# Kernel optimization log

Measured on AMD Instinct MI355X. Metric: run time of the kernel, lower is better.

## Reference

```python
import jax, jax.numpy as jnp
import numpy as np

D_MODEL = 1024
D_HIDDEN = 4096
NUM_BANKS = 16
NUM_SELECTED = 2


def setup_inputs() -> dict:
    key = jax.random.key(0)
    ks = jax.random.split(key, 7)
    s = 0.02
    return {
        "tensor": jax.random.normal(ks[0], (4, 1024, D_MODEL), dtype=jnp.float32),
        "Wr": jax.random.normal(ks[1], (D_MODEL, NUM_BANKS), dtype=jnp.float32) * s,
        "br": jnp.zeros((NUM_BANKS,), dtype=jnp.float32),
        "W1": jax.random.normal(ks[2], (NUM_BANKS, D_MODEL, D_HIDDEN), dtype=jnp.float32) * s,
        "b1": jnp.zeros((NUM_BANKS, D_HIDDEN), dtype=jnp.float32),
        "W2": jax.random.normal(ks[3], (NUM_BANKS, D_HIDDEN, D_MODEL), dtype=jnp.float32) * s,
        "b2": jnp.zeros((NUM_BANKS, D_MODEL), dtype=jnp.float32),
    }


def reference(tensor, Wr, br, W1, b1, W2, b2):
    # Router: softmax over banks, keep top-k probabilities (BankSelector)
    logits = jnp.einsum("bsd,de->bse", tensor, Wr) + br          # [B,S,E]
    probs = jax.nn.softmax(logits, axis=-1)
    topv, topi = jax.lax.top_k(probs, NUM_SELECTED)              # [B,S,K]
    # Dense gate [B,S,E]: selected banks carry their router probability,
    # all other banks are zeroed (equivalent to sparse dispatch/combine).
    gate = jnp.sum(jax.nn.one_hot(topi, NUM_BANKS, dtype=tensor.dtype)
                   * topv[..., None], axis=-2)                    # [B,S,E]
    # Banked expert FFN (BankedLinear x2 with ReLU between)
    h = jax.nn.relu(jnp.einsum("bsd,edh->bseh", tensor, W1) + b1)  # [B,S,E,Dh]
    y = jnp.einsum("bseh,ehm->bsem", h, W2) + b2                   # [B,S,E,Dm]
    # Weighted combine across selected banks
    out = jnp.einsum("bse,bsem->bsm", gate, y)                     # [B,S,Dm]
    return out
```

## Files before the change

kernel.cpp:

```cpp
#include <hip/hip_runtime.h>
#include <stdint.h>

#define D_MODEL   1024
#define D_HIDDEN  4096
#define NBANKS    16
#define NTOK      4096

#define BM 128
#define BN 128
#define BK 32
#define TBUF (BM * BK)
#define KS2 4

typedef __attribute__((ext_vector_type(8))) short bf16x8;
typedef __attribute__((ext_vector_type(4))) float f32x4;
typedef __attribute__((ext_vector_type(4))) unsigned int u32x4;
typedef __attribute__((ext_vector_type(2))) unsigned int u32x2;

__device__ __forceinline__ unsigned short f2bf(float f) {
  unsigned u = __builtin_bit_cast(unsigned, f);
  u += 0x7FFFu + ((u >> 16) & 1u);
  return (unsigned short)(u >> 16);
}

__device__ __forceinline__ unsigned cvtpk(float lo, float hi) {
  unsigned r;
  asm("v_cvt_pk_bf16_f32 %0, %1, %2" : "=v"(r) : "v"(lo), "v"(hi));
  return r;
}

__device__ __forceinline__ int sidx(int r, int k) {
  return (r << 5) + ((((k >> 3) ^ ((r >> 2) & 3)) << 3) | (k & 7));
}

__global__ __launch_bounds__(256) void zero_out_k(float4* __restrict__ out4,
                                                  int* __restrict__ counts) {
  size_t i = (size_t)blockIdx.x * 256 + threadIdx.x;
  out4[i] = make_float4(0.f, 0.f, 0.f, 0.f);
  if (blockIdx.x == 0 && threadIdx.x < NBANKS) counts[threadIdx.x] = 0;
}

__global__ __launch_bounds__(256) void cvtx_k(const float* __restrict__ X,
                                              unsigned short* __restrict__ Xb) {
  const size_t i = ((size_t)blockIdx.x * 256 + threadIdx.x) * 8;
  const float4 a = *(const float4*)(X + i);
  const float4 b = *(const float4*)(X + i + 4);
  u32x4 v;
  v[0] = cvtpk(a.x, a.y); v[1] = cvtpk(a.z, a.w);
  v[2] = cvtpk(b.x, b.y); v[3] = cvtpk(b.z, b.w);
  *(u32x4*)(Xb + i) = v;
}

__global__ __launch_bounds__(64) void router_k(const float* __restrict__ x,
                                               const float* __restrict__ Wr,
                                               const float* __restrict__ br,
                                               int* __restrict__ topIdx,
                                               float* __restrict__ topGate) {
  const int t = blockIdx.x;
  const int l = threadIdx.x;
  const float* xr = x + (size_t)t * D_MODEL;

  float acc[NBANKS];
#pragma unroll
  for (int e = 0; e < NBANKS; ++e) acc[e] = 0.f;

  for (int d = l; d < D_MODEL; d += 64) {
    const float xv = xr[d];
    const float* wrow = Wr + (size_t)d * NBANKS;
#pragma unroll
    for (int e = 0; e < NBANKS; ++e) acc[e] += xv * wrow[e];
  }
#pragma unroll
  for (int e = 0; e < NBANKS; ++e) {
#pragma unroll
    for (int m = 1; m < 64; m <<= 1) acc[e] += __shfl_xor(acc[e], m, 64);
  }
#pragma unroll
  for (int e = 0; e < NBANKS; ++e) acc[e] += br[e];

  if (l == 0) {
    float mx = acc[0];
#pragma unroll
    for (int e = 1; e < NBANKS; ++e) mx = fmaxf(mx, acc[e]);
    float p[NBANKS];
    float s = 0.f;
#pragma unroll
    for (int e = 0; e < NBANKS; ++e) { p[e] = expf(acc[e] - mx); s += p[e]; }
    int i0 = 0; float v0 = p[0];
#pragma unroll
    for (int e = 1; e < NBANKS; ++e) if (p[e] > v0) { v0 = p[e]; i0 = e; }
    int i1 = -1; float v1 = -1.f;
#pragma unroll
    for (int e = 0; e < NBANKS; ++e) if (e != i0 && p[e] > v1) { v1 = p[e]; i1 = e; }
    const float inv = 1.f / s;
    topIdx[2 * t]     = i0;
    topIdx[2 * t + 1] = i1;
    topGate[2 * t]     = v0 * inv;
    topGate[2 * t + 1] = v1 * inv;
  }
}

__global__ __launch_bounds__(256) void build_lists_k(const int* __restrict__ topIdx,
                                                     const float* __restrict__ topGate,
                                                     int* __restrict__ counts,
                                                     int* __restrict__ rowlist,
                                                     float* __restrict__ gatelist) {
  const int t = blockIdx.x * 256 + threadIdx.x;
  if (t >= NTOK) return;
#pragma unroll
  for (int k = 0; k < 2; ++k) {
    const int e = topIdx[2 * t + k];
    const int p = atomicAdd(&counts[e], 1);
    rowlist[e * NTOK + p]  = t;
    gatelist[e * NTOK + p] = topGate[2 * t + k];
  }
}

__global__ void scan_k(const int* __restrict__ counts, int* __restrict__ bankOff) {
  if (threadIdx.x == 0) {
    int s = 0;
#pragma unroll
    for (int e = 0; e < NBANKS; ++e) { bankOff[e] = s; s += counts[e]; }
    bankOff[NBANKS] = s;
  }
}

__global__ __launch_bounds__(256, 2) void gemm1_k(const unsigned short* __restrict__ Xb,
                                                  const float* __restrict__ W1,
                                                  const float* __restrict__ b1,
                                                  const int* __restrict__ counts,
                                                  const int* __restrict__ bankOff,
                                                  const int* __restrict__ rowlist,
                                                  unsigned short* __restrict__ H) {
  const int e   = blockIdx.z;
  const int cnt = counts[e];
  const int m0  = blockIdx.y * BM;
  if (m0 >= cnt) return;
  const int n0  = blockIdx.x * BN;

  const int tid  = threadIdx.x;
  const int lane = tid & 63;
  const int w    = tid >> 6;
  const int wm   = (w >> 1) * 64;
  const int wn   = (w & 1) * 64;

  __shared__ unsigned short Xs[2 * TBUF];
  __shared__ unsigned short Ws[2 * TBUF];

  const int arow = tid >> 1;
  const int ak   = (tid & 1) * 16;
  const int gi   = min(m0 + arow, cnt - 1);
  const int tok  = rowlist[e * NTOK + gi];
  const unsigned short* Asrc = Xb + (size_t)tok * D_MODEL + ak;
  const int xo0 = sidx(arow, ak);
  const int xo1 = sidx(arow, ak + 8);

  const int n4 = 4 * (tid & 31);
  const int k4 = 4 * (tid >> 5);
  const float* Bsrc = W1 + (size_t)e * D_MODEL * D_HIDDEN + (size_t)k4 * D_HIDDEN + n0 + n4;
  int wo[4];
#pragma unroll
  for (int i = 0; i < 4; ++i) wo[i] = sidx(n4 + i, k4);

  const int fr = lane & 15;
  const int fc = (lane >> 4) * 8;
  int aoff[4], boff[4];
#pragma unroll
  for (int i = 0; i < 4; ++i) {
    aoff[i] = sidx(wm + i * 16 + fr, fc);
    boff[i] = sidx(wn + i * 16 + fr, fc);
  }

  bf16x8 ra0, ra1;
  float rbf[4][4];

  f32x4 acc[4][4];
#pragma unroll
  for (int i = 0; i < 4; ++i)
#pragma unroll
    for (int j = 0; j < 4; ++j)
#pragma unroll
      for (int r = 0; r < 4; ++r) acc[i][j][r] = 0.f;

  unsigned short* xc = &Xs[0];       unsigned short* wc = &Ws[0];
  unsigned short* xn = &Xs[TBUF];    unsigned short* wn_ = &Ws[TBUF];

  auto LOAD = [&](int t) {
    const unsigned short* ap = Asrc + t * BK;
    ra0 = *(const bf16x8*)(ap);
    ra1 = *(const bf16x8*)(ap + 8);
    const float* bp = Bsrc + (size_t)t * BK * D_HIDDEN;
#pragma unroll
    for (int kk = 0; kk < 4; ++kk)
      *(float4*)&rbf[kk][0] = *(const float4*)(bp + (size_t)kk * D_HIDDEN);
  };

  auto WRITE = [&](unsigned short* xs, unsigned short* ws) {
    *(bf16x8*)(xs + xo0) = ra0;
    *(bf16x8*)(xs + xo1) = ra1;
#pragma unroll
    for (int i = 0; i < 4; ++i) {
      u32x2 v;
      v[0] = cvtpk(rbf[0][i], rbf[1][i]);
      v[1] = cvtpk(rbf[2][i], rbf[3][i]);
      *(u32x2*)(ws + wo[i]) = v;
    }
  };

  auto COMPUTE = [&](const unsigned short* xs, const unsigned short* ws) {
    bf16x8 af[4], bb[4];
#pragma unroll
    for (int mb = 0; mb < 4; ++mb) af[mb] = *(const bf16x8*)(xs + aoff[mb]);
#pragma unroll
    for (int nb = 0; nb < 4; ++nb) bb[nb] = *(const bf16x8*)(ws + boff[nb]);
#pragma unroll
    for (int mb = 0; mb < 4; ++mb)
#pragma unroll
      for (int nb = 0; nb < 4; ++nb)
        acc[mb][nb] = __builtin_amdgcn_mfma_f32_16x16x32_bf16(af[mb], bb[nb], acc[mb][nb], 0, 0, 0);
  };

  const int NT = D_MODEL / BK;
  LOAD(0);
  WRITE(xc, wc);
  __syncthreads();
#pragma unroll 1
  for (int t = 0; t < NT; ++t) {
    if (t + 1 < NT) LOAD(t + 1);
    __builtin_amdgcn_sched_barrier(0);
    COMPUTE(xc, wc);
    if (t + 1 < NT) WRITE(xn, wn_);
    __syncthreads();
    unsigned short* t0 = xc; xc = xn;  xn  = t0;
    unsigned short* t1 = wc; wc = wn_; wn_ = t1;
  }

  const int hb = bankOff[e] + m0;
  const int rq = (lane >> 4) * 4;
#pragma unroll
  for (int nb = 0; nb < 4; ++nb) {
    const int col = n0 + wn + nb * 16 + fr;
    const float bias = b1[e * D_HIDDEN + col];
#pragma unroll
    for (int mb = 0; mb < 4; ++mb)
#pragma unroll
      for (int r = 0; r < 4; ++r) {
        const int rowT = wm + mb * 16 + rq + r;
        if (m0 + rowT < cnt) {
          float v = acc[mb][nb][r] + bias;
          v = fmaxf(v, 0.f);
          H[(size_t)(hb + rowT) * D_HIDDEN + col] = f2bf(v);
        }
      }
  }
}

__global__ __launch_bounds__(256, 2) void gemm2_k(const unsigned short* __restrict__ H,
                                                  const float* __restrict__ W2,
                                                  const float* __restrict__ b2,
                                                  const int* __restrict__ counts,
                                                  const int* __restrict__ bankOff,
                                                  const int* __restrict__ rowlist,
                                                  const float* __restrict__ gatelist,
                                                  float* __restrict__ out) {
  const int z   = blockIdx.z;
  const int e   = z >> 2;
  const int kc  = z & 3;
  const int cnt = counts[e];
  const int m0  = blockIdx.y * BM;
  if (m0 >= cnt) return;
  const int n0  = blockIdx.x * BN;
  const int kc0 = kc * (D_HIDDEN / KS2);

  const int tid  = threadIdx.x;
  const int lane = tid & 63;
  const int w    = tid >> 6;
  const int wm   = (w >> 1) * 64;
  const int wn   = (w & 1) * 64;

  __shared__ unsigned short Xs[2 * TBUF];
  __shared__ unsigned short Ws[2 * TBUF];

  const int arow = tid >> 1;
  const int ak   = (tid & 1) * 16;
  const int hb   = bankOff[e];
  const int gi   = hb + min(m0 + arow, cnt - 1);
  const unsigned short* Asrc = H + (size_t)gi * D_HIDDEN + kc0 + ak;
  const int xo0 = sidx(arow, ak);
  const int xo1 = sidx(arow, ak + 8);

  const int n4 = 4 * (tid & 31);
  const int k4 = 4 * (tid >> 5);
  const float* Bsrc = W2 + (size_t)e * D_HIDDEN * D_MODEL + (size_t)(kc0 + k4) * D_MODEL + n0 + n4;
  int wo[4];
#pragma unroll
  for (int i = 0; i < 4; ++i) wo[i] = sidx(n4 + i, k4);

  const int fr = lane & 15;
  const int fc = (lane >> 4) * 8;
  int aoff[4], boff[4];
#pragma unroll
  for (int i = 0; i < 4; ++i) {
    aoff[i] = sidx(wm + i * 16 + fr, fc);
    boff[i] = sidx(wn + i * 16 + fr, fc);
  }

  bf16x8 ra0, ra1;
  float rbf[4][4];

  f32x4 acc[4][4];
#pragma unroll
  for (int i = 0; i < 4; ++i)
#pragma unroll
    for (int j = 0; j < 4; ++j)
#pragma unroll
      for (int r = 0; r < 4; ++r) acc[i][j][r] = 0.f;

  unsigned short* xc = &Xs[0];       unsigned short* wc = &Ws[0];
  unsigned short* xn = &Xs[TBUF];    unsigned short* wn_ = &Ws[TBUF];

  auto LOAD = [&](int t) {
    const unsigned short* ap = Asrc + t * BK;
    ra0 = *(const bf16x8*)(ap);
    ra1 = *(const bf16x8*)(ap + 8);
    const float* bp = Bsrc + (size_t)t * BK * D_MODEL;
#pragma unroll
    for (int kk = 0; kk < 4; ++kk)
      *(float4*)&rbf[kk][0] = *(const float4*)(bp + (size_t)kk * D_MODEL);
  };

  auto WRITE = [&](unsigned short* xs, unsigned short* ws) {
    *(bf16x8*)(xs + xo0) = ra0;
    *(bf16x8*)(xs + xo1) = ra1;
#pragma unroll
    for (int i = 0; i < 4; ++i) {
      u32x2 v;
      v[0] = cvtpk(rbf[0][i], rbf[1][i]);
      v[1] = cvtpk(rbf[2][i], rbf[3][i]);
      *(u32x2*)(ws + wo[i]) = v;
    }
  };

  auto COMPUTE = [&](const unsigned short* xs, const unsigned short* ws) {
    bf16x8 af[4], bb[4];
#pragma unroll
    for (int mb = 0; mb < 4; ++mb) af[mb] = *(const bf16x8*)(xs + aoff[mb]);
#pragma unroll
    for (int nb = 0; nb < 4; ++nb) bb[nb] = *(const bf16x8*)(ws + boff[nb]);
#pragma unroll
    for (int mb = 0; mb < 4; ++mb)
#pragma unroll
      for (int nb = 0; nb < 4; ++nb)
        acc[mb][nb] = __builtin_amdgcn_mfma_f32_16x16x32_bf16(af[mb], bb[nb], acc[mb][nb], 0, 0, 0);
  };

  const int NT = (D_HIDDEN / KS2) / BK;
  LOAD(0);
  WRITE(xc, wc);
  __syncthreads();
#pragma unroll 1
  for (int t = 0; t < NT; ++t) {
    if (t + 1 < NT) LOAD(t + 1);
    __builtin_amdgcn_sched_barrier(0);
    COMPUTE(xc, wc);
    if (t + 1 < NT) WRITE(xn, wn_);
    __syncthreads();
    unsigned short* t0 = xc; xc = xn;  xn  = t0;
    unsigned short* t1 = wc; wc = wn_; wn_ = t1;
  }

  const int rq = (lane >> 4) * 4;
  float bias[4];
#pragma unroll
  for (int nb = 0; nb < 4; ++nb)
    bias[nb] = (kc == 0) ? b2[e * D_MODEL + n0 + wn + nb * 16 + fr] : 0.f;

#pragma unroll
  for (int mb = 0; mb < 4; ++mb)
#pragma unroll
    for (int r = 0; r < 4; ++r) {
      const int rowT = wm + mb * 16 + rq + r;
      if (m0 + rowT < cnt) {
        const int si = e * NTOK + m0 + rowT;
        const int tok = rowlist[si];
        const float g = gatelist[si];
        float* orow = out + (size_t)tok * D_MODEL;
#pragma unroll
        for (int nb = 0; nb < 4; ++nb) {
          const int col = n0 + wn + nb * 16 + fr;
          atomicAdd(&orow[col], g * (acc[mb][nb][r] + bias[nb]));
        }
      }
    }
}

extern "C" void kernel_launch(void* const* d_in, const int* in_sizes, int n_in,
                              void* d_out, int out_size, void* d_ws, size_t ws_size,
                              hipStream_t stream) {
  const float* X  = (const float*)d_in[0];
  const float* Wr = (const float*)d_in[1];
  const float* br = (const float*)d_in[2];
  const float* W1 = (const float*)d_in[3];
  const float* b1 = (const float*)d_in[4];
  const float* W2 = (const float*)d_in[5];
  const float* b2 = (const float*)d_in[6];
  float* out = (float*)d_out;

  char* w = (char*)d_ws;
  int*   topIdx   = (int*)(w);
  float* topGate  = (float*)(w + (32 << 10));
  int*   counts   = (int*)(w + (64 << 10));
  int*   bankOff  = (int*)(w + (64 << 10) + 256);
  int*   rowlist  = (int*)(w + (66 << 10));
  float* gatelist = (float*)(w + (66 << 10) + NBANKS * NTOK * 4);
  unsigned short* Xb = (unsigned short*)(w + (1 << 20));
  unsigned short* H  = (unsigned short*)(w + (16 << 20));

  const size_t needed = (size_t)(16 << 20) + (size_t)(NTOK * 2) * D_HIDDEN * 2;
  if (ws_size < needed) return;

  zero_out_k<<<dim3(4096), dim3(256), 0, stream>>>((float4*)out, counts);
  cvtx_k<<<dim3(NTOK * D_MODEL / 8 / 256), dim3(256), 0, stream>>>(X, Xb);
  router_k<<<dim3(NTOK), dim3(64), 0, stream>>>(X, Wr, br, topIdx, topGate);
  build_lists_k<<<dim3(16), dim3(256), 0, stream>>>(topIdx, topGate, counts, rowlist, gatelist);
  scan_k<<<dim3(1), dim3(64), 0, stream>>>(counts, bankOff);
  gemm1_k<<<dim3(D_HIDDEN / BN, NTOK / BM, NBANKS), dim3(256), 0, stream>>>(
      Xb, W1, b1, counts, bankOff, rowlist, H);
  gemm2_k<<<dim3(D_MODEL / BN, NTOK / BM, NBANKS * KS2), dim3(256), 0, stream>>>(
      H, W2, b2, counts, bankOff, rowlist, gatelist, out);
}
```

Baseline: 450.1 us.

## Double K-tile depth, remap blocks across XCDs, and raise MFMA priority

Raises the K tile from 32 to 64 with a new 8-way LDS swizzle, wider 16-byte weight stores and two MFMA sub-steps per tile. This halves the number of barrier iterations per block. The grids are flattened to 1D and block indices are remapped so that consecutive tiles of the same bank land on the same XCD, which should improve L2 reuse of the weights. s_setprio is raised around the MFMA bursts. The larger tiles double LDS use and per-thread staging registers, which could reduce occupancy.

```diff
diff --git a/kernel.cpp b/kernel.cpp
--- a/kernel.cpp
+++ b/kernel.cpp
@@ -8,14 +8,13 @@
 
 #define BM 128
 #define BN 128
-#define BK 32
+#define BK 64
 #define TBUF (BM * BK)
 #define KS2 4
 
 typedef __attribute__((ext_vector_type(8))) short bf16x8;
 typedef __attribute__((ext_vector_type(4))) float f32x4;
 typedef __attribute__((ext_vector_type(4))) unsigned int u32x4;
-typedef __attribute__((ext_vector_type(2))) unsigned int u32x2;
 
 __device__ __forceinline__ unsigned short f2bf(float f) {
   unsigned u = __builtin_bit_cast(unsigned, f);
@@ -30,7 +29,8 @@
 }
 
 __device__ __forceinline__ int sidx(int r, int k) {
-  return (r << 5) + ((((k >> 3) ^ ((r >> 2) & 3)) << 3) | (k & 7));
+  const int x = (((r & 3) << 1) ^ ((r >> 2) & 7)) & 7;
+  return (r << 6) + ((((k >> 3) ^ x) << 3) | (k & 7));
 }
 
 __global__ __launch_bounds__(256) void zero_out_k(float4* __restrict__ out4,
@@ -132,11 +132,15 @@
                                                   const int* __restrict__ bankOff,
                                                   const int* __restrict__ rowlist,
                                                   unsigned short* __restrict__ H) {
-  const int e   = blockIdx.z;
+  const int orig = (blockIdx.x & 7) * 2048 + (blockIdx.x >> 3);
+  const int mI = orig & 31;
+  const int nI = (orig >> 5) & 31;
+  const int e  = orig >> 10;
+
   const int cnt = counts[e];
-  const int m0  = blockIdx.y * BM;
+  const int m0  = mI * BM;
   if (m0 >= cnt) return;
-  const int n0  = blockIdx.x * BN;
+  const int n0  = nI * BN;
 
   const int tid  = threadIdx.x;
   const int lane = tid & 63;
@@ -148,31 +152,35 @@
   __shared__ unsigned short Ws[2 * TBUF];
 
   const int arow = tid >> 1;
-  const int ak   = (tid & 1) * 16;
+  const int ah   = (tid & 1) * 32;
   const int gi   = min(m0 + arow, cnt - 1);
   const int tok  = rowlist[e * NTOK + gi];
-  const unsigned short* Asrc = Xb + (size_t)tok * D_MODEL + ak;
-  const int xo0 = sidx(arow, ak);
-  const int xo1 = sidx(arow, ak + 8);
-
-  const int n4 = 4 * (tid & 31);
-  const int k4 = 4 * (tid >> 5);
-  const float* Bsrc = W1 + (size_t)e * D_MODEL * D_HIDDEN + (size_t)k4 * D_HIDDEN + n0 + n4;
+  const unsigned short* Asrc = Xb + (size_t)tok * D_MODEL + ah;
+  int xo[4];
+#pragma unroll
+  for (int j = 0; j < 4; ++j) xo[j] = sidx(arow, ah + 8 * j);
+
+  const int bu = tid & 31;
+  const int bc = tid >> 5;
+  const float* Bsrc = W1 + (size_t)e * D_MODEL * D_HIDDEN
+                    + (size_t)(8 * bc) * D_HIDDEN + n0 + 4 * bu;
   int wo[4];
 #pragma unroll
-  for (int i = 0; i < 4; ++i) wo[i] = sidx(n4 + i, k4);
+  for (int i = 0; i < 4; ++i) wo[i] = sidx(4 * bu + i, 8 * bc);
 
   const int fr = lane & 15;
-  const int fc = (lane >> 4) * 8;
-  int aoff[4], boff[4];
-#pragma unroll
-  for (int i = 0; i < 4; ++i) {
-    aoff[i] = sidx(wm + i * 16 + fr, fc);
-    boff[i] = sidx(wn + i * 16 + fr, fc);
-  }
-
-  bf16x8 ra0, ra1;
-  float rbf[4][4];
+  const int fg = lane >> 4;
+  int aoff[2][4], boff[2][4];
+#pragma unroll
+  for (int h = 0; h < 2; ++h)
+#pragma unroll
+    for (int i = 0; i < 4; ++i) {
+      aoff[h][i] = sidx(wm + i * 16 + fr, fg * 8 + 32 * h);
+      boff[h][i] = sidx(wn + i * 16 + fr, fg * 8 + 32 * h);
+    }
+
+  bf16x8 ra[4];
+  float rbf[8][4];
 
   f32x4 acc[4][4];
 #pragma unroll
@@ -187,37 +195,44 @@
 
   auto LOAD = [&](int t) {
     const unsigned short* ap = Asrc + t * BK;
-    ra0 = *(const bf16x8*)(ap);
-    ra1 = *(const bf16x8*)(ap + 8);
+#pragma unroll
+    for (int j = 0; j < 4; ++j) ra[j] = *(const bf16x8*)(ap + 8 * j);
     const float* bp = Bsrc + (size_t)t * BK * D_HIDDEN;
 #pragma unroll
-    for (int kk = 0; kk < 4; ++kk)
+    for (int kk = 0; kk < 8; ++kk)
       *(float4*)&rbf[kk][0] = *(const float4*)(bp + (size_t)kk * D_HIDDEN);
   };
 
   auto WRITE = [&](unsigned short* xs, unsigned short* ws) {
-    *(bf16x8*)(xs + xo0) = ra0;
-    *(bf16x8*)(xs + xo1) = ra1;
+#pragma unroll
+    for (int j = 0; j < 4; ++j) *(bf16x8*)(xs + xo[j]) = ra[j];
 #pragma unroll
     for (int i = 0; i < 4; ++i) {
-      u32x2 v;
+      u32x4 v;
       v[0] = cvtpk(rbf[0][i], rbf[1][i]);
       v[1] = cvtpk(rbf[2][i], rbf[3][i]);
-      *(u32x2*)(ws + wo[i]) = v;
+      v[2] = cvtpk(rbf[4][i], rbf[5][i]);
+      v[3] = cvtpk(rbf[6][i], rbf[7][i]);
+      *(u32x4*)(ws + wo[i]) = v;
     }
   };
 
   auto COMPUTE = [&](const unsigned short* xs, const unsigned short* ws) {
-    bf16x8 af[4], bb[4];
-#pragma unroll
-    for (int mb = 0; mb < 4; ++mb) af[mb] = *(const bf16x8*)(xs + aoff[mb]);
-#pragma unroll
-    for (int nb = 0; nb < 4; ++nb) bb[nb] = *(const bf16x8*)(ws + boff[nb]);
-#pragma unroll
-    for (int mb = 0; mb < 4; ++mb)
-#pragma unroll
-      for (int nb = 0; nb < 4; ++nb)
-        acc[mb][nb] = __builtin_amdgcn_mfma_f32_16x16x32_bf16(af[mb], bb[nb], acc[mb][nb], 0, 0, 0);
+#pragma unroll
+    for (int h = 0; h < 2; ++h) {
+      bf16x8 af[4], bb[4];
+#pragma unroll
+      for (int mb = 0; mb < 4; ++mb) af[mb] = *(const bf16x8*)(xs + aoff[h][mb]);
+#pragma unroll
+      for (int nb = 0; nb < 4; ++nb) bb[nb] = *(const bf16x8*)(ws + boff[h][nb]);
+      __builtin_amdgcn_s_setprio(1);
+#pragma unroll
+      for (int mb = 0; mb < 4; ++mb)
+#pragma unroll
+        for (int nb = 0; nb < 4; ++nb)
+          acc[mb][nb] = __builtin_amdgcn_mfma_f32_16x16x32_bf16(af[mb], bb[nb], acc[mb][nb], 0, 0, 0);
+      __builtin_amdgcn_s_setprio(0);
+    }
   };
 
   const int NT = D_MODEL / BK;
@@ -236,7 +251,7 @@
   }
 
   const int hb = bankOff[e] + m0;
-  const int rq = (lane >> 4) * 4;
+  const int rq = fg * 4;
 #pragma unroll
   for (int nb = 0; nb < 4; ++nb) {
     const int col = n0 + wn + nb * 16 + fr;
@@ -263,13 +278,17 @@
                                                   const int* __restrict__ rowlist,
                                                   const float* __restrict__ gatelist,
                                                   float* __restrict__ out) {
-  const int z   = blockIdx.z;
-  const int e   = z >> 2;
-  const int kc  = z & 3;
+  const int orig = (blockIdx.x & 7) * 2048 + (blockIdx.x >> 3);
+  const int mI = orig & 31;
+  const int nI = (orig >> 5) & 7;
+  const int z  = orig >> 8;
+  const int e  = z >> 2;
+  const int kc = z & 3;
+
   const int cnt = counts[e];
-  const int m0  = blockIdx.y * BM;
+  const int m0  = mI * BM;
   if (m0 >= cnt) return;
-  const int n0  = blockIdx.x * BN;
+  const int n0  = nI * BN;
   const int kc0 = kc * (D_HIDDEN / KS2);
 
   const int tid  = threadIdx.x;
@@ -282,31 +301,35 @@
   __shared__ unsigned short Ws[2 * TBUF];
 
   const int arow = tid >> 1;
-  const int ak   = (tid & 1) * 16;
+  const int ah   = (tid & 1) * 32;
   const int hb   = bankOff[e];
   const int gi   = hb + min(m0 + arow, cnt - 1);
-  const unsigned short* Asrc = H + (size_t)gi * D_HIDDEN + kc0 + ak;
-  const int xo0 = sidx(arow, ak);
-  const int xo1 = sidx(arow, ak + 8);
-
-  const int n4 = 4 * (tid & 31);
-  const int k4 = 4 * (tid >> 5);
-  const float* Bsrc = W2 + (size_t)e * D_HIDDEN * D_MODEL + (size_t)(kc0 + k4) * D_MODEL + n0 + n4;
+  const unsigned short* Asrc = H + (size_t)gi * D_HIDDEN + kc0 + ah;
+  int xo[4];
+#pragma unroll
+  for (int j = 0; j < 4; ++j) xo[j] = sidx(arow, ah + 8 * j);
+
+  const int bu = tid & 31;
+  const int bc = tid >> 5;
+  const float* Bsrc = W2 + (size_t)e * D_HIDDEN * D_MODEL
+                    + (size_t)(kc0 + 8 * bc) * D_MODEL + n0 + 4 * bu;
   int wo[4];
 #pragma unroll
-  for (int i = 0; i < 4; ++i) wo[i] = sidx(n4 + i, k4);
+  for (int i = 0; i < 4; ++i) wo[i] = sidx(4 * bu + i, 8 * bc);
 
   const int fr = lane & 15;
-  const int fc = (lane >> 4) * 8;
-  int aoff[4], boff[4];
-#pragma unroll
-  for (int i = 0; i < 4; ++i) {
-    aoff[i] = sidx(wm + i * 16 + fr, fc);
-    boff[i] = sidx(wn + i * 16 + fr, fc);
-  }
-
-  bf16x8 ra0, ra1;
-  float rbf[4][4];
+  const int fg = lane >> 4;
+  int aoff[2][4], boff[2][4];
+#pragma unroll
+  for (int h = 0; h < 2; ++h)
+#pragma unroll
+    for (int i = 0; i < 4; ++i) {
+      aoff[h][i] = sidx(wm + i * 16 + fr, fg * 8 + 32 * h);
+      boff[h][i] = sidx(wn + i * 16 + fr, fg * 8 + 32 * h);
+    }
+
+  bf16x8 ra[4];
+  float rbf[8][4];
 
   f32x4 acc[4][4];
 #pragma unroll
@@ -321,37 +344,44 @@
 
   auto LOAD = [&](int t) {
     const unsigned short* ap = Asrc + t * BK;
-    ra0 = *(const bf16x8*)(ap);
-    ra1 = *(const bf16x8*)(ap + 8);
+#pragma unroll
+    for (int j = 0; j < 4; ++j) ra[j] = *(const bf16x8*)(ap + 8 * j);
     const float* bp = Bsrc + (size_t)t * BK * D_MODEL;
 #pragma unroll
-    for (int kk = 0; kk < 4; ++kk)
+    for (int kk = 0; kk < 8; ++kk)
       *(float4*)&rbf[kk][0] = *(const float4*)(bp + (size_t)kk * D_MODEL);
   };
 
   auto WRITE = [&](unsigned short* xs, unsigned short* ws) {
-    *(bf16x8*)(xs + xo0) = ra0;
-    *(bf16x8*)(xs + xo1) = ra1;
+#pragma unroll
+    for (int j = 0; j < 4; ++j) *(bf16x8*)(xs + xo[j]) = ra[j];
 #pragma unroll
     for (int i = 0; i < 4; ++i) {
-      u32x2 v;
+      u32x4 v;
       v[0] = cvtpk(rbf[0][i], rbf[1][i]);
       v[1] = cvtpk(rbf[2][i], rbf[3][i]);
-      *(u32x2*)(ws + wo[i]) = v;
+      v[2] = cvtpk(rbf[4][i], rbf[5][i]);
+      v[3] = cvtpk(rbf[6][i], rbf[7][i]);
+      *(u32x4*)(ws + wo[i]) = v;
     }
   };
 
   auto COMPUTE = [&](const unsigned short* xs, const unsigned short* ws) {
-    bf16x8 af[4], bb[4];
-#pragma unroll
-    for (int mb = 0; mb < 4; ++mb) af[mb] = *(const bf16x8*)(xs + aoff[mb]);
-#pragma unroll
-    for (int nb = 0; nb < 4; ++nb) bb[nb] = *(const bf16x8*)(ws + boff[nb]);
-#pragma unroll
-    for (int mb = 0; mb < 4; ++mb)
-#pragma unroll
-      for (int nb = 0; nb < 4; ++nb)
-        acc[mb][nb] = __builtin_amdgcn_mfma_f32_16x16x32_bf16(af[mb], bb[nb], acc[mb][nb], 0, 0, 0);
+#pragma unroll
+    for (int h = 0; h < 2; ++h) {
+      bf16x8 af[4], bb[4];
+#pragma unroll
+      for (int mb = 0; mb < 4; ++mb) af[mb] = *(const bf16x8*)(xs + aoff[h][mb]);
+#pragma unroll
+      for (int nb = 0; nb < 4; ++nb) bb[nb] = *(const bf16x8*)(ws + boff[h][nb]);
+      __builtin_amdgcn_s_setprio(1);
+#pragma unroll
+      for (int mb = 0; mb < 4; ++mb)
+#pragma unroll
+        for (int nb = 0; nb < 4; ++nb)
+          acc[mb][nb] = __builtin_amdgcn_mfma_f32_16x16x32_bf16(af[mb], bb[nb], acc[mb][nb], 0, 0, 0);
+      __builtin_amdgcn_s_setprio(0);
+    }
   };
 
   const int NT = (D_HIDDEN / KS2) / BK;
@@ -369,7 +399,7 @@
     unsigned short* t1 = wc; wc = wn_; wn_ = t1;
   }
 
-  const int rq = (lane >> 4) * 4;
+  const int rq = fg * 4;
   float bias[4];
 #pragma unroll
   for (int nb = 0; nb < 4; ++nb)
@@ -424,8 +454,6 @@
   router_k<<<dim3(NTOK), dim3(64), 0, stream>>>(X, Wr, br, topIdx, topGate);
   build_lists_k<<<dim3(16), dim3(256), 0, stream>>>(topIdx, topGate, counts, rowlist, gatelist);
   scan_k<<<dim3(1), dim3(64), 0, stream>>>(counts, bankOff);
-  gemm1_k<<<dim3(D_HIDDEN / BN, NTOK / BM, NBANKS), dim3(256), 0, stream>>>(
-      Xb, W1, b1, counts, bankOff, rowlist, H);
-  gemm2_k<<<dim3(D_MODEL / BN, NTOK / BM, NBANKS * KS2), dim3(256), 0, stream>>>(
-      H, W2, b2, counts, bankOff, rowlist, gatelist, out);
-}
+  gemm1_k<<<dim3(16384), dim3(256), 0, stream>>>(Xb, W1, b1, counts, bankOff, rowlist, H);
+  gemm2_k<<<dim3(16384), dim3(256), 0, stream>>>(H, W2, b2, counts, bankOff, rowlist, gatelist, out);
+}
```

After: 561.0 us. 1.25x slower.

## Enlarge M tile to 256, remap grid for XCD locality, add MFMA priority

Applied to the files above, without the earlier changes.

Doubles the row tile of both expert GEMMs to 256 rows. Each wave now computes a 128x64 sub-tile, so every fp32 weight tile that is loaded and converted is reused across twice as many tokens. It flattens the 3D grid into a 1D launch with an XCD-interleaved block remap, changes the LDS swizzle, reorders the MFMA loop to stream B fragments, and raises wave priority around the MFMA burst. The cost is twice the accumulator registers (128 floats per lane), which may lower occupancy or cause spills. Banks with few tokens may also waste more rows in padded tiles.

```diff
diff --git a/kernel.cpp b/kernel.cpp
--- a/kernel.cpp
+++ b/kernel.cpp
@@ -6,10 +6,11 @@
 #define NBANKS    16
 #define NTOK      4096
 
-#define BM 128
+#define BM 256
 #define BN 128
 #define BK 32
-#define TBUF (BM * BK)
+#define TBX (BM * BK)
+#define TBW (BN * BK)
 #define KS2 4
 
 typedef __attribute__((ext_vector_type(8))) short bf16x8;
@@ -30,7 +31,7 @@
 }
 
 __device__ __forceinline__ int sidx(int r, int k) {
-  return (r << 5) + ((((k >> 3) ^ ((r >> 2) & 3)) << 3) | (k & 7));
+  return (r << 5) + ((((k >> 3) ^ ((r >> 1) & 3)) << 3) | (k & 7));
 }
 
 __global__ __launch_bounds__(256) void zero_out_k(float4* __restrict__ out4,
@@ -132,28 +133,33 @@
                                                   const int* __restrict__ bankOff,
                                                   const int* __restrict__ rowlist,
                                                   unsigned short* __restrict__ H) {
-  const int e   = blockIdx.z;
+  const int orig = (blockIdx.x & 7) * 1024 + (blockIdx.x >> 3);
+  const int mI = orig & 15;
+  const int nI = (orig >> 4) & 31;
+  const int e  = orig >> 9;
+
   const int cnt = counts[e];
-  const int m0  = blockIdx.y * BM;
+  const int m0  = mI * BM;
   if (m0 >= cnt) return;
-  const int n0  = blockIdx.x * BN;
+  const int n0  = nI * BN;
 
   const int tid  = threadIdx.x;
   const int lane = tid & 63;
   const int w    = tid >> 6;
-  const int wm   = (w >> 1) * 64;
+  const int wm   = (w >> 1) * 128;
   const int wn   = (w & 1) * 64;
-
-  __shared__ unsigned short Xs[2 * TBUF];
-  __shared__ unsigned short Ws[2 * TBUF];
-
-  const int arow = tid >> 1;
-  const int ak   = (tid & 1) * 16;
-  const int gi   = min(m0 + arow, cnt - 1);
-  const int tok  = rowlist[e * NTOK + gi];
-  const unsigned short* Asrc = Xb + (size_t)tok * D_MODEL + ak;
-  const int xo0 = sidx(arow, ak);
-  const int xo1 = sidx(arow, ak + 8);
+  const int fr   = lane & 15;
+  const int fg   = lane >> 4;
+
+  __shared__ unsigned short Xs[2 * TBX];
+  __shared__ unsigned short Ws[2 * TBW];
+
+  const int gi  = min(m0 + tid, cnt - 1);
+  const int tok = rowlist[e * NTOK + gi];
+  const unsigned short* Asrc = Xb + (size_t)tok * D_MODEL;
+  int xo[4];
+#pragma unroll
+  for (int j = 0; j < 4; ++j) xo[j] = sidx(tid, 8 * j);
 
   const int n4 = 4 * (tid & 31);
   const int k4 = 4 * (tid >> 5);
@@ -162,33 +168,30 @@
 #pragma unroll
   for (int i = 0; i < 4; ++i) wo[i] = sidx(n4 + i, k4);
 
-  const int fr = lane & 15;
-  const int fc = (lane >> 4) * 8;
-  int aoff[4], boff[4];
-#pragma unroll
-  for (int i = 0; i < 4; ++i) {
-    aoff[i] = sidx(wm + i * 16 + fr, fc);
-    boff[i] = sidx(wn + i * 16 + fr, fc);
-  }
-
-  bf16x8 ra0, ra1;
+  int aoff[8], boff[4];
+#pragma unroll
+  for (int i = 0; i < 8; ++i) aoff[i] = sidx(wm + i * 16 + fr, fg * 8);
+#pragma unroll
+  for (int i = 0; i < 4; ++i) boff[i] = sidx(wn + i * 16 + fr, fg * 8);
+
+  bf16x8 ra[4];
   float rbf[4][4];
 
-  f32x4 acc[4][4];
-#pragma unroll
-  for (int i = 0; i < 4; ++i)
+  f32x4 acc[8][4];
+#pragma unroll
+  for (int i = 0; i < 8; ++i)
 #pragma unroll
     for (int j = 0; j < 4; ++j)
 #pragma unroll
       for (int r = 0; r < 4; ++r) acc[i][j][r] = 0.f;
 
-  unsigned short* xc = &Xs[0];       unsigned short* wc = &Ws[0];
-  unsigned short* xn = &Xs[TBUF];    unsigned short* wn_ = &Ws[TBUF];
+  unsigned short* xc = &Xs[0];     unsigned short* wc = &Ws[0];
+  unsigned short* xn = &Xs[TBX];   unsigned short* wn_ = &Ws[TBW];
 
   auto LOAD = [&](int t) {
     const unsigned short* ap = Asrc + t * BK;
-    ra0 = *(const bf16x8*)(ap);
-    ra1 = *(const bf16x8*)(ap + 8);
+#pragma unroll
+    for (int j = 0; j < 4; ++j) ra[j] = *(const bf16x8*)(ap + 8 * j);
     const float* bp = Bsrc + (size_t)t * BK * D_HIDDEN;
 #pragma unroll
     for (int kk = 0; kk < 4; ++kk)
@@ -196,8 +199,8 @@
   };
 
   auto WRITE = [&](unsigned short* xs, unsigned short* ws) {
-    *(bf16x8*)(xs + xo0) = ra0;
-    *(bf16x8*)(xs + xo1) = ra1;
+#pragma unroll
+    for (int j = 0; j < 4; ++j) *(bf16x8*)(xs + xo[j]) = ra[j];
 #pragma unroll
     for (int i = 0; i < 4; ++i) {
       u32x2 v;
@@ -208,16 +211,18 @@
   };
 
   auto COMPUTE = [&](const unsigned short* xs, const unsigned short* ws) {
-    bf16x8 af[4], bb[4];
-#pragma unroll
-    for (int mb = 0; mb < 4; ++mb) af[mb] = *(const bf16x8*)(xs + aoff[mb]);
-#pragma unroll
-    for (int nb = 0; nb < 4; ++nb) bb[nb] = *(const bf16x8*)(ws + boff[nb]);
-#pragma unroll
-    for (int mb = 0; mb < 4; ++mb)
-#pragma unroll
-      for (int nb = 0; nb < 4; ++nb)
-        acc[mb][nb] = __builtin_amdgcn_mfma_f32_16x16x32_bf16(af[mb], bb[nb], acc[mb][nb], 0, 0, 0);
+    bf16x8 af[8];
+#pragma unroll
+    for (int mb = 0; mb < 8; ++mb) af[mb] = *(const bf16x8*)(xs + aoff[mb]);
+    __builtin_amdgcn_s_setprio(1);
+#pragma unroll
+    for (int nb = 0; nb < 4; ++nb) {
+      const bf16x8 bb = *(const bf16x8*)(ws + boff[nb]);
+#pragma unroll
+      for (int mb = 0; mb < 8; ++mb)
+        acc[mb][nb] = __builtin_amdgcn_mfma_f32_16x16x32_bf16(af[mb], bb, acc[mb][nb], 0, 0, 0);
+    }
+    __builtin_amdgcn_s_setprio(0);
   };
 
   const int NT = D_MODEL / BK;
@@ -236,13 +241,13 @@
   }
 
   const int hb = bankOff[e] + m0;
-  const int rq = (lane >> 4) * 4;
+  const int rq = fg * 4;
 #pragma unroll
   for (int nb = 0; nb < 4; ++nb) {
     const int col = n0 + wn + nb * 16 + fr;
     const float bias = b1[e * D_HIDDEN + col];
 #pragma unroll
-    for (int mb = 0; mb < 4; ++mb)
+    for (int mb = 0; mb < 8; ++mb)
 #pragma unroll
       for (int r = 0; r < 4; ++r) {
         const int rowT = wm + mb * 16 + rq + r;
@@ -263,31 +268,36 @@
                                                   const int* __restrict__ rowlist,
                                                   const float* __restrict__ gatelist,
                                                   float* __restrict__ out) {
-  const int z   = blockIdx.z;
-  const int e   = z >> 2;
-  const int kc  = z & 3;
+  const int orig = (blockIdx.x & 7) * 1024 + (blockIdx.x >> 3);
+  const int mI = orig & 15;
+  const int nI = (orig >> 4) & 7;
+  const int z  = orig >> 7;
+  const int e  = z >> 2;
+  const int kc = z & 3;
+
   const int cnt = counts[e];
-  const int m0  = blockIdx.y * BM;
+  const int m0  = mI * BM;
   if (m0 >= cnt) return;
-  const int n0  = blockIdx.x * BN;
+  const int n0  = nI * BN;
   const int kc0 = kc * (D_HIDDEN / KS2);
 
   const int tid  = threadIdx.x;
   const int lane = tid & 63;
   const int w    = tid >> 6;
-  const int wm   = (w >> 1) * 64;
+  const int wm   = (w >> 1) * 128;
   const int wn   = (w & 1) * 64;
-
-  __shared__ unsigned short Xs[2 * TBUF];
-  __shared__ unsigned short Ws[2 * TBUF];
-
-  const int arow = tid >> 1;
-  const int ak   = (tid & 1) * 16;
-  const int hb   = bankOff[e];
-  const int gi   = hb + min(m0 + arow, cnt - 1);
-  const unsigned short* Asrc = H + (size_t)gi * D_HIDDEN + kc0 + ak;
-  const int xo0 = sidx(arow, ak);
-  const int xo1 = sidx(arow, ak + 8);
+  const int fr   = lane & 15;
+  const int fg   = lane >> 4;
+
+  __shared__ unsigned short Xs[2 * TBX];
+  __shared__ unsigned short Ws[2 * TBW];
+
+  const int hb = bankOff[e];
+  const int gi = hb + min(m0 + tid, cnt - 1);
+  const unsigned short* Asrc = H + (size_t)gi * D_HIDDEN + kc0;
+  int xo[4];
+#pragma unroll
+  for (int j = 0; j < 4; ++j) xo[j] = sidx(tid, 8 * j);
 
   const int n4 = 4 * (tid & 31);
   const int k4 = 4 * (tid >> 5);
@@ -296,33 +306,30 @@
 #pragma unroll
   for (int i = 0; i < 4; ++i) wo[i] = sidx(n4 + i, k4);
 
-  const int fr = lane & 15;
-  const int fc = (lane >> 4) * 8;
-  int aoff[4], boff[4];
-#pragma unroll
-  for (int i = 0; i < 4; ++i) {
-    aoff[i] = sidx(wm + i * 16 + fr, fc);
-    boff[i] = sidx(wn + i * 16 + fr, fc);
-  }
-
-  bf16x8 ra0, ra1;
+  int aoff[8], boff[4];
+#pragma unroll
+  for (int i = 0; i < 8; ++i) aoff[i] = sidx(wm + i * 16 + fr, fg * 8);
+#pragma unroll
+  for (int i = 0; i < 4; ++i) boff[i] = sidx(wn + i * 16 + fr, fg * 8);
+
+  bf16x8 ra[4];
   float rbf[4][4];
 
-  f32x4 acc[4][4];
-#pragma unroll
-  for (int i = 0; i < 4; ++i)
+  f32x4 acc[8][4];
+#pragma unroll
+  for (int i = 0; i < 8; ++i)
 #pragma unroll
     for (int j = 0; j < 4; ++j)
 #pragma unroll
       for (int r = 0; r < 4; ++r) acc[i][j][r] = 0.f;
 
-  unsigned short* xc = &Xs[0];       unsigned short* wc = &Ws[0];
-  unsigned short* xn = &Xs[TBUF];    unsigned short* wn_ = &Ws[TBUF];
+  unsigned short* xc = &Xs[0];     unsigned short* wc = &Ws[0];
+  unsigned short* xn = &Xs[TBX];   unsigned short* wn_ = &Ws[TBW];
 
   auto LOAD = [&](int t) {
     const unsigned short* ap = Asrc + t * BK;
-    ra0 = *(const bf16x8*)(ap);
-    ra1 = *(const bf16x8*)(ap + 8);
+#pragma unroll
+    for (int j = 0; j < 4; ++j) ra[j] = *(const bf16x8*)(ap + 8 * j);
     const float* bp = Bsrc + (size_t)t * BK * D_MODEL;
 #pragma unroll
     for (int kk = 0; kk < 4; ++kk)
@@ -330,8 +337,8 @@
   };
 
   auto WRITE = [&](unsigned short* xs, unsigned short* ws) {
-    *(bf16x8*)(xs + xo0) = ra0;
-    *(bf16x8*)(xs + xo1) = ra1;
+#pragma unroll
+    for (int j = 0; j < 4; ++j) *(bf16x8*)(xs + xo[j]) = ra[j];
 #pragma unroll
     for (int i = 0; i < 4; ++i) {
       u32x2 v;
@@ -342,16 +349,18 @@
   };
 
   auto COMPUTE = [&](const unsigned short* xs, const unsigned short* ws) {
-    bf16x8 af[4], bb[4];
-#pragma unroll
-    for (int mb = 0; mb < 4; ++mb) af[mb] = *(const bf16x8*)(xs + aoff[mb]);
-#pragma unroll
-    for (int nb = 0; nb < 4; ++nb) bb[nb] = *(const bf16x8*)(ws + boff[nb]);
-#pragma unroll
-    for (int mb = 0; mb < 4; ++mb)
-#pragma unroll
-      for (int nb = 0; nb < 4; ++nb)
-        acc[mb][nb] = __builtin_amdgcn_mfma_f32_16x16x32_bf16(af[mb], bb[nb], acc[mb][nb], 0, 0, 0);
+    bf16x8 af[8];
+#pragma unroll
+    for (int mb = 0; mb < 8; ++mb) af[mb] = *(const bf16x8*)(xs + aoff[mb]);
+    __builtin_amdgcn_s_setprio(1);
+#pragma unroll
+    for (int nb = 0; nb < 4; ++nb) {
+      const bf16x8 bb = *(const bf16x8*)(ws + boff[nb]);
+#pragma unroll
+      for (int mb = 0; mb < 8; ++mb)
+        acc[mb][nb] = __builtin_amdgcn_mfma_f32_16x16x32_bf16(af[mb], bb, acc[mb][nb], 0, 0, 0);
+    }
+    __builtin_amdgcn_s_setprio(0);
   };
 
   const int NT = (D_HIDDEN / KS2) / BK;
@@ -369,14 +378,14 @@
     unsigned short* t1 = wc; wc = wn_; wn_ = t1;
   }
 
-  const int rq = (lane >> 4) * 4;
+  const int rq = fg * 4;
   float bias[4];
 #pragma unroll
   for (int nb = 0; nb < 4; ++nb)
     bias[nb] = (kc == 0) ? b2[e * D_MODEL + n0 + wn + nb * 16 + fr] : 0.f;
 
 #pragma unroll
-  for (int mb = 0; mb < 4; ++mb)
+  for (int mb = 0; mb < 8; ++mb)
 #pragma unroll
     for (int r = 0; r < 4; ++r) {
       const int rowT = wm + mb * 16 + rq + r;
@@ -424,8 +433,6 @@
   router_k<<<dim3(NTOK), dim3(64), 0, stream>>>(X, Wr, br, topIdx, topGate);
   build_lists_k<<<dim3(16), dim3(256), 0, stream>>>(topIdx, topGate, counts, rowlist, gatelist);
   scan_k<<<dim3(1), dim3(64), 0, stream>>>(counts, bankOff);
-  gemm1_k<<<dim3(D_HIDDEN / BN, NTOK / BM, NBANKS), dim3(256), 0, stream>>>(
-      Xb, W1, b1, counts, bankOff, rowlist, H);
-  gemm2_k<<<dim3(D_MODEL / BN, NTOK / BM, NBANKS * KS2), dim3(256), 0, stream>>>(
-      H, W2, b2, counts, bankOff, rowlist, gatelist, out);
-}
+  gemm1_k<<<dim3(8192), dim3(256), 0, stream>>>(Xb, W1, b1, counts, bankOff, rowlist, H);
+  gemm2_k<<<dim3(8192), dim3(256), 0, stream>>>(H, W2, b2, counts, bankOff, rowlist, gatelist, out);
+}
```

After: 663.5 us. 1.47x slower.

## Load activation tiles directly into LDS and remap grid for XCD locality

Applied to the files above, without the earlier changes.

The activation (A) tile loads in both expert GEMMs now use global_load_lds to copy 16-byte chunks straight into shared memory, with the LDS swizzle changed to match. This drops the register round-trip and the LDS write instructions for A. The 3D grid is flattened to 1D and remapped so that consecutive blocks of one bank/tile group go to the same XCD, which should improve L2 reuse of weights. MFMA sections are also wrapped in s_setprio to raise wave priority during compute. The main risk is correctness of the LDS swizzle and synchronisation ordering, since the async LDS loads depend on the existing __syncthreads with no explicit vmcnt wait.

```diff
diff --git a/kernel.cpp b/kernel.cpp
--- a/kernel.cpp
+++ b/kernel.cpp
@@ -29,8 +29,14 @@
   return r;
 }
 
+__device__ __forceinline__ void glds16(const unsigned short* g, unsigned short* l) {
+  __builtin_amdgcn_global_load_lds(
+      (const __attribute__((address_space(1))) unsigned int*)(const void*)g,
+      (__attribute__((address_space(3))) unsigned int*)(void*)l, 16, 0, 0);
+}
+
 __device__ __forceinline__ int sidx(int r, int k) {
-  return (r << 5) + ((((k >> 3) ^ ((r >> 2) & 3)) << 3) | (k & 7));
+  return (r << 5) + ((((k >> 3) ^ ((r >> 1) & 3)) << 3) | (k & 7));
 }
 
 __global__ __launch_bounds__(256) void zero_out_k(float4* __restrict__ out4,
@@ -132,28 +138,39 @@
                                                   const int* __restrict__ bankOff,
                                                   const int* __restrict__ rowlist,
                                                   unsigned short* __restrict__ H) {
-  const int e   = blockIdx.z;
+  const int orig = (blockIdx.x & 7) * 2048 + (blockIdx.x >> 3);
+  const int mI = orig & 31;
+  const int nI = (orig >> 5) & 31;
+  const int e  = orig >> 10;
+
   const int cnt = counts[e];
-  const int m0  = blockIdx.y * BM;
+  const int m0  = mI * BM;
   if (m0 >= cnt) return;
-  const int n0  = blockIdx.x * BN;
+  const int n0  = nI * BN;
 
   const int tid  = threadIdx.x;
   const int lane = tid & 63;
   const int w    = tid >> 6;
   const int wm   = (w >> 1) * 64;
   const int wn   = (w & 1) * 64;
+  const int fr   = lane & 15;
+  const int fg   = lane >> 4;
 
   __shared__ unsigned short Xs[2 * TBUF];
   __shared__ unsigned short Ws[2 * TBUF];
 
-  const int arow = tid >> 1;
-  const int ak   = (tid & 1) * 16;
-  const int gi   = min(m0 + arow, cnt - 1);
-  const int tok  = rowlist[e * NTOK + gi];
-  const unsigned short* Asrc = Xb + (size_t)tok * D_MODEL + ak;
-  const int xo0 = sidx(arow, ak);
-  const int xo1 = sidx(arow, ak + 8);
+  const unsigned short* agp[2];
+  int albase[2];
+#pragma unroll
+  for (int c = 0; c < 2; ++c) {
+    const int q   = 2 * w + c;
+    const int row = 16 * q + (lane >> 2);
+    const int gi  = min(m0 + row, cnt - 1);
+    const int tok = rowlist[e * NTOK + gi];
+    const int kc_ = (lane & 3) ^ ((row >> 1) & 3);
+    agp[c]    = Xb + (size_t)tok * D_MODEL + 8 * kc_;
+    albase[c] = q * 512;
+  }
 
   const int n4 = 4 * (tid & 31);
   const int k4 = 4 * (tid >> 5);
@@ -162,16 +179,13 @@
 #pragma unroll
   for (int i = 0; i < 4; ++i) wo[i] = sidx(n4 + i, k4);
 
-  const int fr = lane & 15;
-  const int fc = (lane >> 4) * 8;
   int aoff[4], boff[4];
 #pragma unroll
   for (int i = 0; i < 4; ++i) {
-    aoff[i] = sidx(wm + i * 16 + fr, fc);
-    boff[i] = sidx(wn + i * 16 + fr, fc);
-  }
-
-  bf16x8 ra0, ra1;
+    aoff[i] = sidx(wm + i * 16 + fr, fg * 8);
+    boff[i] = sidx(wn + i * 16 + fr, fg * 8);
+  }
+
   float rbf[4][4];
 
   f32x4 acc[4][4];
@@ -185,19 +199,17 @@
   unsigned short* xc = &Xs[0];       unsigned short* wc = &Ws[0];
   unsigned short* xn = &Xs[TBUF];    unsigned short* wn_ = &Ws[TBUF];
 
-  auto LOAD = [&](int t) {
-    const unsigned short* ap = Asrc + t * BK;
-    ra0 = *(const bf16x8*)(ap);
-    ra1 = *(const bf16x8*)(ap + 8);
+  auto GLDSA = [&](unsigned short* xs, int t) {
+    glds16(agp[0] + t * BK, xs + albase[0]);
+    glds16(agp[1] + t * BK, xs + albase[1]);
+  };
+  auto LOADB = [&](int t) {
     const float* bp = Bsrc + (size_t)t * BK * D_HIDDEN;
 #pragma unroll
     for (int kk = 0; kk < 4; ++kk)
       *(float4*)&rbf[kk][0] = *(const float4*)(bp + (size_t)kk * D_HIDDEN);
   };
-
-  auto WRITE = [&](unsigned short* xs, unsigned short* ws) {
-    *(bf16x8*)(xs + xo0) = ra0;
-    *(bf16x8*)(xs + xo1) = ra1;
+  auto WRITEB = [&](unsigned short* ws) {
 #pragma unroll
     for (int i = 0; i < 4; ++i) {
       u32x2 v;
@@ -206,37 +218,39 @@
       *(u32x2*)(ws + wo[i]) = v;
     }
   };
-
   auto COMPUTE = [&](const unsigned short* xs, const unsigned short* ws) {
     bf16x8 af[4], bb[4];
 #pragma unroll
     for (int mb = 0; mb < 4; ++mb) af[mb] = *(const bf16x8*)(xs + aoff[mb]);
 #pragma unroll
     for (int nb = 0; nb < 4; ++nb) bb[nb] = *(const bf16x8*)(ws + boff[nb]);
+    __builtin_amdgcn_s_setprio(1);
 #pragma unroll
     for (int mb = 0; mb < 4; ++mb)
 #pragma unroll
       for (int nb = 0; nb < 4; ++nb)
         acc[mb][nb] = __builtin_amdgcn_mfma_f32_16x16x32_bf16(af[mb], bb[nb], acc[mb][nb], 0, 0, 0);
+    __builtin_amdgcn_s_setprio(0);
   };
 
   const int NT = D_MODEL / BK;
-  LOAD(0);
-  WRITE(xc, wc);
+  GLDSA(xc, 0);
+  LOADB(0);
+  WRITEB(wc);
   __syncthreads();
 #pragma unroll 1
   for (int t = 0; t < NT; ++t) {
-    if (t + 1 < NT) LOAD(t + 1);
+    if (t + 1 < NT) { GLDSA(xn, t + 1); LOADB(t + 1); }
     __builtin_amdgcn_sched_barrier(0);
     COMPUTE(xc, wc);
-    if (t + 1 < NT) WRITE(xn, wn_);
+    if (t + 1 < NT) WRITEB(wn_);
     __syncthreads();
     unsigned short* t0 = xc; xc = xn;  xn  = t0;
     unsigned short* t1 = wc; wc = wn_; wn_ = t1;
   }
 
   const int hb = bankOff[e] + m0;
-  const int rq = (lane >> 4) * 4;
+  const int rq = fg * 4;
 #pragma unroll
   for (int nb = 0; nb < 4; ++nb) {
     const int col = n0 + wn + nb * 16 + fr;
@@ -263,13 +277,17 @@
                                                   const int* __restrict__ rowlist,
                                                   const float* __restrict__ gatelist,
                                                   float* __restrict__ out) {
-  const int z   = blockIdx.z;
-  const int e   = z >> 2;
-  const int kc  = z & 3;
+  const int orig = (blockIdx.x & 7) * 2048 + (blockIdx.x >> 3);
+  const int mI = orig & 31;
+  const int nI = (orig >> 5) & 7;
+  const int z  = orig >> 8;
+  const int e  = z >> 2;
+  const int kc = z & 3;
+
   const int cnt = counts[e];
-  const int m0  = blockIdx.y * BM;
+  const int m0  = mI * BM;
   if (m0 >= cnt) return;
-  const int n0  = blockIdx.x * BN;
+  const int n0  = nI * BN;
   const int kc0 = kc * (D_HIDDEN / KS2);
 
   const int tid  = threadIdx.x;
@@ -277,17 +295,24 @@
   const int w    = tid >> 6;
   const int wm   = (w >> 1) * 64;
   const int wn   = (w & 1) * 64;
+  const int fr   = lane & 15;
+  const int fg   = lane >> 4;
 
   __shared__ unsigned short Xs[2 * TBUF];
   __shared__ unsigned short Ws[2 * TBUF];
 
-  const int arow = tid >> 1;
-  const int ak   = (tid & 1) * 16;
-  const int hb   = bankOff[e];
-  const int gi   = hb + min(m0 + arow, cnt - 1);
-  const unsigned short* Asrc = H + (size_t)gi * D_HIDDEN + kc0 + ak;
-  const int xo0 = sidx(arow, ak);
-  const int xo1 = sidx(arow, ak + 8);
+  const int hb = bankOff[e];
+  const unsigned short* agp[2];
+  int albase[2];
+#pragma unroll
+  for (int c = 0; c < 2; ++c) {
+    const int q   = 2 * w + c;
+    const int row = 16 * q + (lane >> 2);
+    const int gi  = hb + min(m0 + row, cnt - 1);
+    const int kc_ = (lane & 3) ^ ((row >> 1) & 3);
+    agp[c]    = H + (size_t)gi * D_HIDDEN + kc0 + 8 * kc_;
+    albase[c] = q * 512;
+  }
 
   const int n4 = 4 * (tid & 31);
   const int k4 = 4 * (tid >> 5);
@@ -296,16 +321,13 @@
 #pragma unroll
   for (int i = 0; i < 4; ++i) wo[i] = sidx(n4 + i, k4);
 
-  const int fr = lane & 15;
-  const int fc = (lane >> 4) * 8;
   int aoff[4], boff[4];
 #pragma unroll
   for (int i = 0; i < 4; ++i) {
-    aoff[i] = sidx(wm + i * 16 + fr, fc);
-    boff[i] = sidx(wn + i * 16 + fr, fc);
-  }
-
-  bf16x8 ra0, ra1;
+    aoff[i] = sidx(wm + i * 16 + fr, fg * 8);
+    boff[i] = sidx(wn + i * 16 + fr, fg * 8);
+  }
+
   float rbf[4][4];
 
   f32x4 acc[4][4];
@@ -319,19 +341,17 @@
   unsigned short* xc = &Xs[0];       unsigned short* wc = &Ws[0];
   unsigned short* xn = &Xs[TBUF];    unsigned short* wn_ = &Ws[TBUF];
 
-  auto LOAD = [&](int t) {
-    const unsigned short* ap = Asrc + t * BK;
-    ra0 = *(const bf16x8*)(ap);
-    ra1 = *(const bf16x8*)(ap + 8);
+  auto GLDSA = [&](unsigned short* xs, int t) {
+    glds16(agp[0] + t * BK, xs + albase[0]);
+    glds16(agp[1] + t * BK, xs + albase[1]);
+  };
+  auto LOADB = [&](int t) {
     const float* bp = Bsrc + (size_t)t * BK * D_MODEL;
 #pragma unroll
     for (int kk = 0; kk < 4; ++kk)
       *(float4*)&rbf[kk][0] = *(const float4*)(bp + (size_t)kk * D_MODEL);
   };
-
-  auto WRITE = [&](unsigned short* xs, unsigned short* ws) {
-    *(bf16x8*)(xs + xo0) = ra0;
-    *(bf16x8*)(xs + xo1) = ra1;
+  auto WRITEB = [&](unsigned short* ws) {
 #pragma unroll
     for (int i = 0; i < 4; ++i) {
       u32x2 v;
@@ -340,36 +360,38 @@
       *(u32x2*)(ws + wo[i]) = v;
     }
   };
-
   auto COMPUTE = [&](const unsigned short* xs, const unsigned short* ws) {
     bf16x8 af[4], bb[4];
 #pragma unroll
     for (int mb = 0; mb < 4; ++mb) af[mb] = *(const bf16x8*)(xs + aoff[mb]);
 #pragma unroll
     for (int nb = 0; nb < 4; ++nb) bb[nb] = *(const bf16x8*)(ws + boff[nb]);
+    __builtin_amdgcn_s_setprio(1);
 #pragma unroll
     for (int mb = 0; mb < 4; ++mb)
 #pragma unroll
       for (int nb = 0; nb < 4; ++nb)
         acc[mb][nb] = __builtin_amdgcn_mfma_f32_16x16x32_bf16(af[mb], bb[nb], acc[mb][nb], 0, 0, 0);
+    __builtin_amdgcn_s_setprio(0);
   };
 
   const int NT = (D_HIDDEN / KS2) / BK;
-  LOAD(0);
-  WRITE(xc, wc);
+  GLDSA(xc, 0);
+  LOADB(0);
+  WRITEB(wc);
   __syncthreads();
 #pragma unroll 1
   for (int t = 0; t < NT; ++t) {
-    if (t + 1 < NT) LOAD(t + 1);
+    if (t + 1 < NT) { GLDSA(xn, t + 1); LOADB(t + 1); }
     __builtin_amdgcn_sched_barrier(0);
     COMPUTE(xc, wc);
-    if (t + 1 < NT) WRITE(xn, wn_);
+    if (t + 1 < NT) WRITEB(wn_);
     __syncthreads();
     unsigned short* t0 = xc; xc = xn;  xn  = t0;
     unsigned short* t1 = wc; wc = wn_; wn_ = t1;
   }
 
-  const int rq = (lane >> 4) * 4;
+  const int rq = fg * 4;
   float bias[4];
 #pragma unroll
   for (int nb = 0; nb < 4; ++nb)
@@ -424,8 +446,6 @@
   router_k<<<dim3(NTOK), dim3(64), 0, stream>>>(X, Wr, br, topIdx, topGate);
   build_lists_k<<<dim3(16), dim3(256), 0, stream>>>(topIdx, topGate, counts, rowlist, gatelist);
   scan_k<<<dim3(1), dim3(64), 0, stream>>>(counts, bankOff);
-  gemm1_k<<<dim3(D_HIDDEN / BN, NTOK / BM, NBANKS), dim3(256), 0, stream>>>(
-      Xb, W1, b1, counts, bankOff, rowlist, H);
-  gemm2_k<<<dim3(D_MODEL / BN, NTOK / BM, NBANKS * KS2), dim3(256), 0, stream>>>(
-      H, W2, b2, counts, bankOff, rowlist, gatelist, out);
-}
+  gemm1_k<<<dim3(16384), dim3(256), 0, stream>>>(Xb, W1, b1, counts, bankOff, rowlist, H);
+  gemm2_k<<<dim3(16384), dim3(256), 0, stream>>>(H, W2, b2, counts, bankOff, rowlist, gatelist, out);
+}
```

Measured after the change: 607.4 us. +34.9%, slower.
